# Kernel optimization log

Hardware: AMD Instinct MI355X
Metric: run time of the kernel (lower is better)

The kernel has to match this reference:

```python
import jax, jax.numpy as jnp
import numpy as np

EMBED_DIM = 2048
NUM_HEADS = 16
HEAD_DIM = EMBED_DIM // NUM_HEADS
SCALES = [(1, 1, 1), (1, 2, 2), (1, 4, 4), (1, 6, 6), (1, 8, 8),
          (1, 12, 12), (1, 16, 16), (1, 20, 20), (1, 24, 24), (1, 32, 32)]
LENS = [t * h * w for (t, h, w) in SCALES]
SEQ_LEN = int(np.sum(LENS))  # 2521
BATCH = 2
MAX_SCALE_MUL = float(np.log(100.0))


def _block_causal_bias():
    # VAR-style: queries in scale-block i attend to all keys up to end of block i.
    cum = np.cumsum(LENS)
    q_end = np.repeat(cum, LENS)                      # [L] visible kv length per query
    visible = np.arange(SEQ_LEN)[None, :] < q_end[:, None]
    bias = np.where(visible, 0.0, -np.inf).astype(np.float32)
    return jnp.asarray(bias)[None, None]              # [1,1,L,L]


def setup_inputs() -> dict:
    key = jax.random.key(0)
    ks = jax.random.split(key, 8)
    C, H, hd, L, B = EMBED_DIM, NUM_HEADS, HEAD_DIM, SEQ_LEN, BATCH
    x = jax.random.normal(ks[0], (B, L, C), dtype=jnp.float32)
    W_qkv = jax.random.normal(ks[1], (3 * C, C), dtype=jnp.float32) * (1.0 / np.sqrt(C))
    q_bias = jnp.zeros((C,), jnp.float32)
    v_bias = jnp.zeros((C,), jnp.float32)
    scale_mul_log = jnp.full((1, H, 1, 1), np.log(4.0), jnp.float32)
    proj_W = jax.random.normal(ks[2], (C, C), dtype=jnp.float32) * (1.0 / np.sqrt(C))
    proj_b = jnp.zeros((C,), jnp.float32)
    # 2D RoPE cache, pre-sliced for scale_ind=0: (2,1,1,1,L,hd//2) = (cos, sin)
    angles = jax.random.uniform(ks[3], (L, hd // 2), dtype=jnp.float32, maxval=2.0 * np.pi)
    rope_cache = jnp.stack([jnp.cos(angles), jnp.sin(angles)])[:, None, None, None]
    attn_bias = _block_causal_bias()
    return {"x": x, "W_qkv": W_qkv, "q_bias": q_bias, "v_bias": v_bias,
            "scale_mul_log": scale_mul_log, "proj_W": proj_W, "proj_b": proj_b,
            "rope_cache": rope_cache, "attn_bias": attn_bias}


def _l2norm(t, eps=1e-12):
    # torch F.normalize: x / max(||x||_2, eps)
    n = jnp.sqrt(jnp.sum(t * t, axis=-1, keepdims=True))
    return t / jnp.maximum(n, eps)


def reference(x, W_qkv, q_bias, v_bias, scale_mul_log, proj_W, proj_b, rope_cache, attn_bias):
    B, L, C = x.shape
    H, hd = NUM_HEADS, HEAD_DIM
    bias = jnp.concatenate([q_bias, jnp.zeros_like(q_bias), v_bias])
    qkv = x @ W_qkv.T + bias                               # [B,L,3C]
    qkv = qkv.reshape(B, L, 3, H, hd).transpose(2, 0, 3, 1, 4)  # [3,B,H,L,hd]
    q, k, v = qkv[0], qkv[1], qkv[2]
    # cosine attention: L2-norm q,k; q scaled by clamped learnable per-head scale
    scale_mul = jnp.exp(jnp.minimum(scale_mul_log, MAX_SCALE_MUL))
    q = _l2norm(q) * scale_mul
    k = _l2norm(k)
    # 2D RoPE applied jointly to q and k
    qk = jnp.stack([q, k]).reshape(2, B, H, L, hd // 2, 2)
    cos, sin = rope_cache[0], rope_cache[1]                # [1,1,1,L,hd//2]
    re = cos * qk[..., 0] - sin * qk[..., 1]
    im = sin * qk[..., 0] + cos * qk[..., 1]
    qk = jnp.stack([re, im], axis=-1).reshape(2, B, H, L, hd)
    q, k = qk[0], qk[1]
    # SDPA with scale=1 (cos_attn) and additive block-causal bias
    scores = jnp.einsum('bhqd,bhkd->bhqk', q, k) + attn_bias
    attn = jax.nn.softmax(scores, axis=-1)
    out = jnp.einsum('bhqk,bhkd->bhqd', attn, v)           # [B,H,L,hd]
    out = out.transpose(0, 2, 1, 3).reshape(B, L, C)
    return out @ proj_W.T + proj_b
```

## Files before the change

### kernel.cpp

```cpp
#include <hip/hip_runtime.h>
#include <stdint.h>

#define SEQL 2521
#define LPAD 2560
#define NB 2
#define NH 16
#define HD 128
#define CD 2048
#define KD 2048

typedef float f32x4 __attribute__((ext_vector_type(4)));
typedef __bf16 bf16x8 __attribute__((ext_vector_type(8)));
typedef unsigned short u16x8 __attribute__((ext_vector_type(8)));

static __device__ __forceinline__ unsigned short bf16c(float f){
  __bf16 h = (__bf16)f;
  return __builtin_bit_cast(unsigned short, h);
}
static __device__ __forceinline__ float bf2f(unsigned short s){
  union { unsigned u; float f; } v; v.u = ((unsigned)s) << 16; return v.f;
}
static __device__ __forceinline__ bf16x8 asbf(u16x8 v){ return __builtin_bit_cast(bf16x8, v); }

typedef const __attribute__((address_space(1))) unsigned int* gas1_t;
typedef __attribute__((address_space(3))) unsigned int* las3_t;
static __device__ __forceinline__ void glds16(const void* g, void* l){
  __builtin_amdgcn_global_load_lds((gas1_t)g, (las3_t)l, 16, 0, 0);
}

__global__ __launch_bounds__(256) void prep_kernel(
    const float* __restrict__ x, const float* __restrict__ wqkv, const float* __restrict__ projw,
    unsigned short* __restrict__ xb, unsigned short* __restrict__ wb, unsigned short* __restrict__ pw)
{
  const int NX = (NB*LPAD*CD)/4;
  const int NW = (3*CD*CD)/4;
  const int NPj = (CD*CD)/4;
  const int total = NX + NW + NPj;
  for (int v = blockIdx.x*256 + threadIdx.x; v < total; v += gridDim.x*256){
    if (v < NX){
      int e = v << 2;
      int row = e >> 11, col = e & 2047;
      int b = (row >= LPAD) ? 1 : 0;
      int l = row - b*LPAD;
      ushort4 o;
      if (l < SEQL){
        const float4 f = *(const float4*)(x + (((long)(b*SEQL + l)) << 11) + col);
        o.x = bf16c(f.x); o.y = bf16c(f.y); o.z = bf16c(f.z); o.w = bf16c(f.w);
      } else { o.x = 0; o.y = 0; o.z = 0; o.w = 0; }
      *(ushort4*)(xb + e) = o;
    } else if (v < NX + NW){
      long i = (long)(v - NX) << 2;
      const float4 f = *(const float4*)(wqkv + i);
      ushort4 o; o.x=bf16c(f.x); o.y=bf16c(f.y); o.z=bf16c(f.z); o.w=bf16c(f.w);
      *(ushort4*)(wb + i) = o;
    } else {
      long i = (long)(v - NX - NW) << 2;
      const float4 f = *(const float4*)(projw + i);
      ushort4 o; o.x=bf16c(f.x); o.y=bf16c(f.y); o.z=bf16c(f.z); o.w=bf16c(f.w);
      *(ushort4*)(pw + i) = o;
    }
  }
}

static __device__ __forceinline__ void gemm_core(
    const unsigned short* __restrict__ A, const unsigned short* __restrict__ Bm,
    unsigned short* As, unsigned short* Bs, int m0, int n0, f32x4 acc[4][4])
{
  const int tid = threadIdx.x;
  const int w = tid >> 6, lane = tid & 63;
  const int g = lane >> 4, lr = lane & 15;
  const int wm = w >> 1, wn = w & 1;
  const unsigned short* aS0 = A + (long)(m0 + (tid >> 2))*KD + ((tid & 3) << 3);
  const unsigned short* aS1 = aS0 + (long)64*KD;
  const unsigned short* bS0 = Bm + (long)(n0 + (tid >> 2))*KD + ((tid & 3) << 3);
  const unsigned short* bS1 = bS0 + (long)64*KD;
  unsigned short* aD0 = As + (w << 9);
  unsigned short* aD1 = As + 2048 + (w << 9);
  unsigned short* bD0 = Bs + (w << 9);
  unsigned short* bD1 = Bs + 2048 + (w << 9);
  const unsigned short* aRd = As + ((wm << 6) + lr)*32 + (g << 3);
  const unsigned short* bRd = Bs + ((wn << 6) + lr)*32 + (g << 3);
  for (int kt = 0; kt < KD/32; ++kt){
    __syncthreads();
    const int ko = kt << 5;
    glds16(aS0 + ko, aD0);
    glds16(aS1 + ko, aD1);
    glds16(bS0 + ko, bD0);
    glds16(bS1 + ko, bD1);
    __syncthreads();
    u16x8 af[4], bfr[4];
#pragma unroll
    for (int i = 0; i < 4; ++i) af[i]  = *(const u16x8*)(aRd + i*16*32);
#pragma unroll
    for (int j = 0; j < 4; ++j) bfr[j] = *(const u16x8*)(bRd + j*16*32);
#pragma unroll
    for (int i = 0; i < 4; ++i)
#pragma unroll
      for (int j = 0; j < 4; ++j)
        acc[i][j] = __builtin_amdgcn_mfma_f32_16x16x32_bf16(asbf(af[i]), asbf(bfr[j]), acc[i][j], 0, 0, 0);
  }
}

__global__ __launch_bounds__(256) void gemm_qkv(
    const unsigned short* __restrict__ A, const unsigned short* __restrict__ W,
    const float* __restrict__ qb, const float* __restrict__ vb,
    unsigned short* __restrict__ qg, unsigned short* __restrict__ kg,
    unsigned short* __restrict__ vt)
{
  __shared__ __align__(16) unsigned short As[128*32];
  __shared__ __align__(16) unsigned short Bs[128*32];
  f32x4 acc[4][4] = {};
  const int m0 = blockIdx.x << 7, n0 = blockIdx.y << 7;
  gemm_core(A, W, As, Bs, m0, n0, acc);
  const int tid = threadIdx.x;
  const int w = tid >> 6, lane = tid & 63, g = lane >> 4, lr = lane & 15;
  const int wm = w >> 1, wn = w & 1;
  const int part = n0 >> 11;
  const int b = (m0 >= LPAD) ? 1 : 0;
  const int l0 = m0 - b*LPAD;
  const int hb = (n0 & 2047) >> 7;
#pragma unroll
  for (int ai = 0; ai < 4; ++ai){
#pragma unroll
    for (int bj = 0; bj < 4; ++bj){
      const int d = (wn << 6) + (bj << 4) + lr;
      const int mloc = (wm << 6) + (ai << 4) + (g << 2);
      const float bias = (part == 0) ? qb[(hb << 7) + d] : ((part == 2) ? vb[(hb << 7) + d] : 0.f);
      const f32x4 v = acc[ai][bj];
      if (part == 2){
        ushort4 o;
        o.x = bf16c(v[0] + bias); o.y = bf16c(v[1] + bias);
        o.z = bf16c(v[2] + bias); o.w = bf16c(v[3] + bias);
        *(ushort4*)(vt + ((long)((b*NH + hb)*HD + d))*LPAD + l0 + mloc) = o;
      } else {
        unsigned short* dst = (part ? kg : qg) + (((long)(b*NH + hb)*LPAD) + l0 + mloc)*HD + d;
        dst[0]     = bf16c(v[0] + bias);
        dst[HD]    = bf16c(v[1] + bias);
        dst[2*HD]  = bf16c(v[2] + bias);
        dst[3*HD]  = bf16c(v[3] + bias);
      }
    }
  }
}

__global__ __launch_bounds__(256) void gemm_proj(
    const unsigned short* __restrict__ A, const unsigned short* __restrict__ W,
    const float* __restrict__ pbias, float* __restrict__ out)
{
  __shared__ __align__(16) unsigned short As[128*32];
  __shared__ __align__(16) unsigned short Bs[128*32];
  f32x4 acc[4][4] = {};
  const int m0 = blockIdx.x << 7, n0 = blockIdx.y << 7;
  gemm_core(A, W, As, Bs, m0, n0, acc);
  const int tid = threadIdx.x;
  const int w = tid >> 6, lane = tid & 63, g = lane >> 4, lr = lane & 15;
  const int wm = w >> 1, wn = w & 1;
  const int b = (m0 >= LPAD) ? 1 : 0;
  const int l0 = m0 - b*LPAD;
#pragma unroll
  for (int ai = 0; ai < 4; ++ai){
#pragma unroll
    for (int bj = 0; bj < 4; ++bj){
      const int n = n0 + (wn << 6) + (bj << 4) + lr;
      const int mloc = (wm << 6) + (ai << 4) + (g << 2);
      const float bias = pbias[n];
      const f32x4 v = acc[ai][bj];
#pragma unroll
      for (int r = 0; r < 4; ++r){
        const int l = l0 + mloc + r;
        if (l < SEQL) out[(((long)b*SEQL + l) << 11) + n] = v[r] + bias;
      }
    }
  }
}

__global__ __launch_bounds__(256) void rope_norm(
    unsigned short* __restrict__ qg, unsigned short* __restrict__ kg,
    const float* __restrict__ rope, const float* __restrict__ smlog)
{
  const int sub = threadIdx.x & 15;
  const int l = blockIdx.x*16 + (threadIdx.x >> 4);
  if (l >= SEQL) return;
  const int pb = blockIdx.y;
  const int part = pb >> 5, bh = pb & 31, h = bh & 15;
  unsigned short* base = (part ? kg : qg) + ((long)bh*LPAD + l)*HD + (sub << 3);
  const u16x8 v = *(const u16x8*)base;
  float f[8];
#pragma unroll
  for (int i = 0; i < 8; ++i) f[i] = bf2f(v[i]);
  float ss = 0.f;
#pragma unroll
  for (int i = 0; i < 8; ++i) ss += f[i]*f[i];
  ss += __shfl_xor(ss, 1, 16);
  ss += __shfl_xor(ss, 2, 16);
  ss += __shfl_xor(ss, 4, 16);
  ss += __shfl_xor(ss, 8, 16);
  float inv = 1.f / fmaxf(sqrtf(ss), 1e-12f);
  if (part == 0){
    float sl = fminf(smlog[h], 4.605170185988091f);
    inv *= __expf(sl) * 1.4426950408889634f;
  }
  const float4 cs = *(const float4*)(rope + (long)l*64 + (sub << 2));
  const float4 sn = *(const float4*)(rope + (long)(SEQL + l)*64 + (sub << 2));
  u16x8 o;
  const float c4[4] = {cs.x, cs.y, cs.z, cs.w};
  const float s4[4] = {sn.x, sn.y, sn.z, sn.w};
#pragma unroll
  for (int p = 0; p < 4; ++p){
    const float re = f[2*p], im = f[2*p+1];
    o[2*p]   = bf16c((c4[p]*re - s4[p]*im)*inv);
    o[2*p+1] = bf16c((s4[p]*re + c4[p]*im)*inv);
  }
  *(u16x8*)base = o;
}

static __device__ __forceinline__ int q_end_of(int q){
  if (q >= SEQL) return 1;
  if (q < 121){
    if (q < 1) return 1;
    if (q < 5) return 5;
    if (q < 21) return 21;
    if (q < 57) return 57;
    return 121;
  }
  if (q < 265) return 265;
  if (q < 521) return 521;
  if (q < 921) return 921;
  if (q < 1497) return 1497;
  return 2521;
}

__global__ __launch_bounds__(512) void attn_kernel(
    const unsigned short* __restrict__ qg, const unsigned short* __restrict__ kg,
    const unsigned short* __restrict__ vt, unsigned short* __restrict__ aout)
{
  __shared__ __align__(16) unsigned short Ks[64*128];
  __shared__ __align__(16) unsigned short Vs[128*64];
  __shared__ __align__(16) unsigned short Ps[8][16*72];
  const int tid = threadIdx.x, w = tid >> 6, lane = tid & 63;
  const int g = lane >> 4, lr = lane & 15;
  const int qt = (int)gridDim.x - 1 - (int)blockIdx.x;
  const int bh = blockIdx.y;
  const int q0 = qt << 7, qw = q0 + (w << 4);
  const long kvBase = (long)bh * LPAD * HD;

  u16x8 qf[4];
  {
    const unsigned short* qrow = qg + kvBase + (long)(qw + lr)*HD + (g << 3);
#pragma unroll
    for (int c = 0; c < 4; ++c) qf[c] = *(const u16x8*)(qrow + (c << 5));
  }
  const int qe  = q_end_of(qw + lr);
  const int qe0 = q_end_of(qw);
  const int qmax = (q0 + 127 < SEQL - 1) ? q0 + 127 : SEQL - 1;
  const int nt = (q_end_of(qmax) + 63) >> 6;

  float m2 = -1e30f, l_run = 0.f;
  f32x4 acco[8] = {};

  for (int t = 0; t < nt; ++t){
    __syncthreads();
    const int kvb = t << 6;
#pragma unroll
    for (int c = 0; c < 2; ++c){
      const int idx = (c << 9) + tid;
      const int kv = idx >> 4, ch = idx & 15;
      glds16(kg + kvBase + (long)(kvb + kv)*HD + ((ch ^ (kv & 7)) << 3),
             Ks + (c << 12) + (w << 9));
      const int dd = idx >> 3, ch2 = idx & 7;
      glds16(vt + kvBase + (long)dd*LPAD + kvb + ((ch2 ^ (dd & 7)) << 3),
             Vs + (c << 12) + (w << 9));
    }
    __syncthreads();

    f32x4 accs[4] = {};
    __builtin_amdgcn_s_setprio(1);
#pragma unroll
    for (int mf = 0; mf < 4; ++mf){
      const int kvr = (mf << 4) + lr;
      const unsigned short* krow = Ks + kvr*HD;
      const int sw = kvr & 7;
#pragma unroll
      for (int c = 0; c < 4; ++c){
        u16x8 kf = *(const u16x8*)(krow + ((((c << 2) + g) ^ sw) << 3));
        accs[mf] = __builtin_amdgcn_mfma_f32_16x16x32_bf16(asbf(kf), asbf(qf[c]), accs[mf], 0, 0, 0);
      }
    }
    __builtin_amdgcn_s_setprio(0);

    float tmax = -1e30f;
    if (kvb + 64 <= qe0){
#pragma unroll
      for (int mf = 0; mf < 4; ++mf)
#pragma unroll
        for (int r = 0; r < 4; ++r) tmax = fmaxf(tmax, accs[mf][r]);
    } else {
#pragma unroll
      for (int mf = 0; mf < 4; ++mf){
#pragma unroll
        for (int r = 0; r < 4; ++r){
          const int kvg = kvb + (mf << 4) + (g << 2) + r;
          float s = (kvg < qe) ? accs[mf][r] : -1e30f;
          accs[mf][r] = s;
          tmax = fmaxf(tmax, s);
        }
      }
    }
    tmax = fmaxf(tmax, __shfl_xor(tmax, 16, 64));
    tmax = fmaxf(tmax, __shfl_xor(tmax, 32, 64));

    float alpha = 1.f;
    const bool need = !__all(tmax <= m2 + 11.0f);
    if (need){
      const float mnew = fmaxf(m2, tmax);
      alpha = exp2f(m2 - mnew);
      m2 = mnew;
      const float a0 = __shfl(alpha, (g << 2) + 0, 64);
      const float a1 = __shfl(alpha, (g << 2) + 1, 64);
      const float a2 = __shfl(alpha, (g << 2) + 2, 64);
      const float a3 = __shfl(alpha, (g << 2) + 3, 64);
#pragma unroll
      for (int nf = 0; nf < 8; ++nf){
        acco[nf][0] *= a0; acco[nf][1] *= a1; acco[nf][2] *= a2; acco[nf][3] *= a3;
      }
    }

    float tsum = 0.f;
#pragma unroll
    for (int mf = 0; mf < 4; ++mf){
#pragma unroll
      for (int r = 0; r < 4; ++r){
        const float p = exp2f(accs[mf][r] - m2);
        accs[mf][r] = p;
        tsum += p;
      }
    }
    tsum += __shfl_xor(tsum, 16, 64);
    tsum += __shfl_xor(tsum, 32, 64);
    l_run = l_run*alpha + tsum;

    unsigned short* prow = &Ps[w][lr*72 + (g << 2)];
#pragma unroll
    for (int mf = 0; mf < 4; ++mf){
      uint2 pk;
      pk.x = (unsigned)bf16c(accs[mf][0]) | ((unsigned)bf16c(accs[mf][1]) << 16);
      pk.y = (unsigned)bf16c(accs[mf][2]) | ((unsigned)bf16c(accs[mf][3]) << 16);
      *(uint2*)(prow + (mf << 4)) = pk;
    }

    __builtin_amdgcn_s_setprio(1);
#pragma unroll
    for (int c = 0; c < 2; ++c){
      u16x8 pf = *(const u16x8*)(&Ps[w][lr*72 + (c << 5) + (g << 3)]);
      const int sw2 = lr & 7;
#pragma unroll
      for (int nf = 0; nf < 8; ++nf){
        u16x8 vf = *(const u16x8*)(Vs + ((nf << 4) + lr)*64 + ((((c << 2) + g) ^ sw2) << 3));
        acco[nf] = __builtin_amdgcn_mfma_f32_16x16x32_bf16(asbf(pf), asbf(vf), acco[nf], 0, 0, 0);
      }
    }
    __builtin_amdgcn_s_setprio(0);
  }

  const float rcp = 1.f / l_run;
  const float li0 = __shfl(rcp, (g << 2) + 0, 64);
  const float li1 = __shfl(rcp, (g << 2) + 1, 64);
  const float li2 = __shfl(rcp, (g << 2) + 2, 64);
  const float li3 = __shfl(rcp, (g << 2) + 3, 64);
  const int b = bh >> 4, h = bh & 15;
#pragma unroll
  for (int r = 0; r < 4; ++r){
    const int qq = qw + (g << 2) + r;
    if (qq < SEQL){
      const float lir = (r == 0) ? li0 : ((r == 1) ? li1 : ((r == 2) ? li2 : li3));
      unsigned short* dst = aout + (((long)(b*LPAD + qq)) << 11) + (h << 7) + lr;
#pragma unroll
      for (int nf = 0; nf < 8; ++nf)
        dst[nf << 4] = bf16c(acco[nf][r] * lir);
    }
  }
}

extern "C" void kernel_launch(void* const* d_in, const int* in_sizes, int n_in,
                              void* d_out, int out_size, void* d_ws, size_t ws_size,
                              hipStream_t stream) {
  const float* x     = (const float*)d_in[0];
  const float* wqkv  = (const float*)d_in[1];
  const float* qb    = (const float*)d_in[2];
  const float* vb    = (const float*)d_in[3];
  const float* smlog = (const float*)d_in[4];
  const float* projw = (const float*)d_in[5];
  const float* projb = (const float*)d_in[6];
  const float* rope  = (const float*)d_in[7];
  float* out = (float*)d_out;

  unsigned short* xb = (unsigned short*)d_ws;
  unsigned short* wb = xb + (size_t)NB*LPAD*CD;
  unsigned short* pw = wb + (size_t)3*CD*CD;
  unsigned short* qg = pw + (size_t)CD*CD;
  unsigned short* kg = qg + (size_t)NB*NH*LPAD*HD;
  unsigned short* vt = kg + (size_t)NB*NH*LPAD*HD;

  prep_kernel<<<2048, 256, 0, stream>>>(x, wqkv, projw, xb, wb, pw);
  gemm_qkv<<<dim3(40, 48), 256, 0, stream>>>(xb, wb, qb, vb, qg, kg, vt);
  rope_norm<<<dim3(158, 64), 256, 0, stream>>>(qg, kg, rope, smlog);
  attn_kernel<<<dim3(20, 32), 512, 0, stream>>>(qg, kg, vt, xb);
  gemm_proj<<<dim3(40, 16), 256, 0, stream>>>(xb, pw, projb, out);
}
```

Before: 574.2 us.

## Rewrite QKV and projection GEMMs as 256x256 double-buffered pipelined 8-wave kernels

Replaces the simple 128x128 GEMM core, which issues two block-wide barriers per 32-wide k step, with a 256x256-tile, 512-thread kernel. It uses a double-buffered 64-wide k stage, XOR-swizzled LDS layout, interleaved global-to-LDS loads between MFMA phases, and s_setprio around the MFMA bursts. A swizzled 1D block index groups neighbouring tiles for L2 reuse. The aim is to hide load latency and raise MFMA utilisation, at the cost of 128KB LDS per block, large accumulators, and fewer blocks (160 for proj), which may cut occupancy and wave-level parallelism.

```diff
diff --git a/kernel.cpp b/kernel.cpp
--- a/kernel.cpp
+++ b/kernel.cpp
@@ -62,78 +62,154 @@
   }
 }
 
-static __device__ __forceinline__ void gemm_core(
+static __device__ __forceinline__ void gemm8p(
     const unsigned short* __restrict__ A, const unsigned short* __restrict__ Bm,
-    unsigned short* As, unsigned short* Bs, int m0, int n0, f32x4 acc[4][4])
+    unsigned short* lds, int m0, int n0, f32x4 acc[8][4])
 {
   const int tid = threadIdx.x;
   const int w = tid >> 6, lane = tid & 63;
   const int g = lane >> 4, lr = lane & 15;
-  const int wm = w >> 1, wn = w & 1;
-  const unsigned short* aS0 = A + (long)(m0 + (tid >> 2))*KD + ((tid & 3) << 3);
-  const unsigned short* aS1 = aS0 + (long)64*KD;
-  const unsigned short* bS0 = Bm + (long)(n0 + (tid >> 2))*KD + ((tid & 3) << 3);
-  const unsigned short* bS1 = bS0 + (long)64*KD;
-  unsigned short* aD0 = As + (w << 9);
-  unsigned short* aD1 = As + 2048 + (w << 9);
-  unsigned short* bD0 = Bs + (w << 9);
-  unsigned short* bD1 = Bs + 2048 + (w << 9);
-  const unsigned short* aRd = As + ((wm << 6) + lr)*32 + (g << 3);
-  const unsigned short* bRd = Bs + ((wn << 6) + lr)*32 + (g << 3);
-  for (int kt = 0; kt < KD/32; ++kt){
-    __syncthreads();
-    const int ko = kt << 5;
-    glds16(aS0 + ko, aD0);
-    glds16(aS1 + ko, aD1);
-    glds16(bS0 + ko, bD0);
-    glds16(bS1 + ko, bD1);
-    __syncthreads();
-    u16x8 af[4], bfr[4];
-#pragma unroll
-    for (int i = 0; i < 4; ++i) af[i]  = *(const u16x8*)(aRd + i*16*32);
-#pragma unroll
-    for (int j = 0; j < 4; ++j) bfr[j] = *(const u16x8*)(bRd + j*16*32);
-#pragma unroll
-    for (int i = 0; i < 4; ++i)
-#pragma unroll
-      for (int j = 0; j < 4; ++j)
-        acc[i][j] = __builtin_amdgcn_mfma_f32_16x16x32_bf16(asbf(af[i]), asbf(bfr[j]), acc[i][j], 0, 0, 0);
-  }
-}
-
-__global__ __launch_bounds__(256) void gemm_qkv(
+  const int wm = w >> 2, wn = w & 3;
+  const int xorv = (lr & 7) << 3;
+  const int off0 = (g << 3) ^ xorv;
+  const int arow = wm*128 + lr;
+  const int brow = wn*64 + lr;
+
+  auto stage = [&](int mat, int kt, int half, int buf){
+    const unsigned short* G = mat ? Bm : A;
+    const int base0 = mat ? n0 : m0;
+    unsigned short* lb = lds + buf*32768 + mat*16384;
+#pragma unroll
+    for (int p = 0; p < 2; ++p){
+      const int cb_ = (half<<10) + (p<<9) + (w<<6);
+      const int c = cb_ + lane;
+      const int row = c >> 3, cc = c & 7;
+      glds16(G + (size_t)(base0 + row)*KD + (kt<<6) + ((cc ^ (row & 7)) << 3),
+             lb + (cb_ << 3));
+    }
+  };
+  auto rdA = [&](int buf, int i, int ks)->u16x8 {
+    return *(const u16x8*)(lds + buf*32768 + (arow + i*16)*64 + (off0 ^ (ks<<5)));
+  };
+  auto rdB = [&](int buf, int j, int ks)->u16x8 {
+    return *(const u16x8*)(lds + buf*32768 + 16384 + (brow + j*16)*64 + (off0 ^ (ks<<5)));
+  };
+
+  u16x8 bfr[4][2], af[2][2];
+  auto mfma16 = [&](int q){
+#pragma unroll
+    for (int i2 = 0; i2 < 2; ++i2)
+#pragma unroll
+      for (int ks = 0; ks < 2; ++ks)
+#pragma unroll
+        for (int j = 0; j < 4; ++j)
+          acc[2*q+i2][j] = __builtin_amdgcn_mfma_f32_16x16x32_bf16(
+              asbf(af[i2][ks]), asbf(bfr[j][ks]), acc[2*q+i2][j], 0, 0, 0);
+  };
+
+#define PH_SYNC_MFMA(Q) \
+    __builtin_amdgcn_s_barrier(); \
+    asm volatile("s_waitcnt lgkmcnt(0)" ::: "memory"); \
+    __builtin_amdgcn_s_setprio(1); mfma16(Q); __builtin_amdgcn_s_setprio(0);
+
+  stage(0, 0, 0, 0); stage(0, 0, 1, 0);
+  stage(1, 0, 0, 0); stage(1, 0, 1, 0);
+  stage(1, 1, 0, 1); stage(1, 1, 1, 1);
+  asm volatile("s_waitcnt vmcnt(4)" ::: "memory");
+  __builtin_amdgcn_s_barrier();
+
+  const int NI = KD >> 7;
+  for (int it = 0; it < NI; ++it){
+    const int kt = it << 1;
+    const bool last = (it == NI-1);
+#pragma unroll
+    for (int j = 0; j < 4; ++j){ bfr[j][0]=rdB(0,j,0); bfr[j][1]=rdB(0,j,1); }
+    af[0][0]=rdA(0,0,0); af[0][1]=rdA(0,0,1); af[1][0]=rdA(0,1,0); af[1][1]=rdA(0,1,1);
+    stage(0, kt+1, 0, 1);
+    PH_SYNC_MFMA(0)
+    __builtin_amdgcn_s_barrier();
+
+    af[0][0]=rdA(0,2,0); af[0][1]=rdA(0,2,1); af[1][0]=rdA(0,3,0); af[1][1]=rdA(0,3,1);
+    stage(0, kt+1, 1, 1);
+    PH_SYNC_MFMA(1)
+    __builtin_amdgcn_s_barrier();
+
+    af[0][0]=rdA(0,4,0); af[0][1]=rdA(0,4,1); af[1][0]=rdA(0,5,0); af[1][1]=rdA(0,5,1);
+    if (!last) stage(1, kt+2, 0, 0);
+    PH_SYNC_MFMA(2)
+    __builtin_amdgcn_s_barrier();
+
+    af[0][0]=rdA(0,6,0); af[0][1]=rdA(0,6,1); af[1][0]=rdA(0,7,0); af[1][1]=rdA(0,7,1);
+    if (!last) stage(1, kt+2, 1, 0);
+    PH_SYNC_MFMA(3)
+    if (last) { asm volatile("s_waitcnt vmcnt(0)" ::: "memory"); }
+    else      { asm volatile("s_waitcnt vmcnt(4)" ::: "memory"); }
+    __builtin_amdgcn_s_barrier();
+
+#pragma unroll
+    for (int j = 0; j < 4; ++j){ bfr[j][0]=rdB(1,j,0); bfr[j][1]=rdB(1,j,1); }
+    af[0][0]=rdA(1,0,0); af[0][1]=rdA(1,0,1); af[1][0]=rdA(1,1,0); af[1][1]=rdA(1,1,1);
+    if (!last) stage(0, kt+2, 0, 0);
+    PH_SYNC_MFMA(0)
+    __builtin_amdgcn_s_barrier();
+
+    af[0][0]=rdA(1,2,0); af[0][1]=rdA(1,2,1); af[1][0]=rdA(1,3,0); af[1][1]=rdA(1,3,1);
+    if (!last) stage(0, kt+2, 1, 0);
+    PH_SYNC_MFMA(1)
+    __builtin_amdgcn_s_barrier();
+
+    af[0][0]=rdA(1,4,0); af[0][1]=rdA(1,4,1); af[1][0]=rdA(1,5,0); af[1][1]=rdA(1,5,1);
+    if (!last) stage(1, kt+3, 0, 1);
+    PH_SYNC_MFMA(2)
+    __builtin_amdgcn_s_barrier();
+
+    af[0][0]=rdA(1,6,0); af[0][1]=rdA(1,6,1); af[1][0]=rdA(1,7,0); af[1][1]=rdA(1,7,1);
+    if (!last) stage(1, kt+3, 1, 1);
+    PH_SYNC_MFMA(3)
+    if (last) { asm volatile("s_waitcnt vmcnt(0)" ::: "memory"); }
+    else      { asm volatile("s_waitcnt vmcnt(4)" ::: "memory"); }
+    __builtin_amdgcn_s_barrier();
+  }
+#undef PH_SYNC_MFMA
+}
+
+__global__ __launch_bounds__(512, 2) void gemm_qkv(
     const unsigned short* __restrict__ A, const unsigned short* __restrict__ W,
     const float* __restrict__ qb, const float* __restrict__ vb,
     unsigned short* __restrict__ qg, unsigned short* __restrict__ kg,
     unsigned short* __restrict__ vt)
 {
-  __shared__ __align__(16) unsigned short As[128*32];
-  __shared__ __align__(16) unsigned short Bs[128*32];
-  f32x4 acc[4][4] = {};
-  const int m0 = blockIdx.x << 7, n0 = blockIdx.y << 7;
-  gemm_core(A, W, As, Bs, m0, n0, acc);
+  __shared__ __align__(16) unsigned short lds[65536];
+  f32x4 acc[8][4] = {};
+  const int bid = blockIdx.x;
+  const int swz = (bid & 7)*60 + (bid >> 3);
+  const int mt = swz / 24, ntt = swz % 24;
+  const int m0 = mt << 8, n0 = ntt << 8;
+  gemm8p(A, W, lds, m0, n0, acc);
+
   const int tid = threadIdx.x;
   const int w = tid >> 6, lane = tid & 63, g = lane >> 4, lr = lane & 15;
-  const int wm = w >> 1, wn = w & 1;
+  const int wm = w >> 2, wn = w & 3;
   const int part = n0 >> 11;
   const int b = (m0 >= LPAD) ? 1 : 0;
   const int l0 = m0 - b*LPAD;
-  const int hb = (n0 & 2047) >> 7;
-#pragma unroll
-  for (int ai = 0; ai < 4; ++ai){
-#pragma unroll
-    for (int bj = 0; bj < 4; ++bj){
-      const int d = (wn << 6) + (bj << 4) + lr;
-      const int mloc = (wm << 6) + (ai << 4) + (g << 2);
-      const float bias = (part == 0) ? qb[(hb << 7) + d] : ((part == 2) ? vb[(hb << 7) + d] : 0.f);
-      const f32x4 v = acc[ai][bj];
+  const int colbase = (n0 & 2047) + wn*64;
+#pragma unroll
+  for (int i = 0; i < 8; ++i){
+    const int mloc = wm*128 + i*16 + (g << 2);
+#pragma unroll
+    for (int j = 0; j < 4; ++j){
+      const int col = colbase + j*16 + lr;
+      const int hb = col >> 7, d = col & 127;
+      const float bias = (part == 0) ? qb[col] : ((part == 2) ? vb[col] : 0.f);
+      const f32x4 v = acc[i][j];
       if (part == 2){
         ushort4 o;
         o.x = bf16c(v[0] + bias); o.y = bf16c(v[1] + bias);
         o.z = bf16c(v[2] + bias); o.w = bf16c(v[3] + bias);
-        *(ushort4*)(vt + ((long)((b*NH + hb)*HD + d))*LPAD + l0 + mloc) = o;
+        *(ushort4*)(vt + ((size_t)((b*NH + hb)*HD + d))*LPAD + l0 + mloc) = o;
       } else {
-        unsigned short* dst = (part ? kg : qg) + (((long)(b*NH + hb)*LPAD) + l0 + mloc)*HD + d;
+        unsigned short* dst = (part ? kg : qg) + (((size_t)(b*NH + hb)*LPAD) + l0 + mloc)*HD + d;
         dst[0]     = bf16c(v[0] + bias);
         dst[HD]    = bf16c(v[1] + bias);
         dst[2*HD]  = bf16c(v[2] + bias);
@@ -143,32 +219,35 @@
   }
 }
 
-__global__ __launch_bounds__(256) void gemm_proj(
+__global__ __launch_bounds__(512, 2) void gemm_proj(
     const unsigned short* __restrict__ A, const unsigned short* __restrict__ W,
     const float* __restrict__ pbias, float* __restrict__ out)
 {
-  __shared__ __align__(16) unsigned short As[128*32];
-  __shared__ __align__(16) unsigned short Bs[128*32];
-  f32x4 acc[4][4] = {};
-  const int m0 = blockIdx.x << 7, n0 = blockIdx.y << 7;
-  gemm_core(A, W, As, Bs, m0, n0, acc);
+  __shared__ __align__(16) unsigned short lds[65536];
+  f32x4 acc[8][4] = {};
+  const int bid = blockIdx.x;
+  const int swz = (bid & 7)*20 + (bid >> 3);
+  const int mt = swz >> 3, ntt = swz & 7;
+  const int m0 = mt << 8, n0 = ntt << 8;
+  gemm8p(A, W, lds, m0, n0, acc);
+
   const int tid = threadIdx.x;
   const int w = tid >> 6, lane = tid & 63, g = lane >> 4, lr = lane & 15;
-  const int wm = w >> 1, wn = w & 1;
+  const int wm = w >> 2, wn = w & 3;
   const int b = (m0 >= LPAD) ? 1 : 0;
   const int l0 = m0 - b*LPAD;
 #pragma unroll
-  for (int ai = 0; ai < 4; ++ai){
-#pragma unroll
-    for (int bj = 0; bj < 4; ++bj){
-      const int n = n0 + (wn << 6) + (bj << 4) + lr;
-      const int mloc = (wm << 6) + (ai << 4) + (g << 2);
+  for (int i = 0; i < 8; ++i){
+    const int mloc = wm*128 + i*16 + (g << 2);
+#pragma unroll
+    for (int j = 0; j < 4; ++j){
+      const int n = n0 + wn*64 + j*16 + lr;
       const float bias = pbias[n];
-      const f32x4 v = acc[ai][bj];
+      const f32x4 v = acc[i][j];
 #pragma unroll
       for (int r = 0; r < 4; ++r){
         const int l = l0 + mloc + r;
-        if (l < SEQL) out[(((long)b*SEQL + l) << 11) + n] = v[r] + bias;
+        if (l < SEQL) out[(((size_t)(b*SEQL + l)) << 11) + n] = v[r] + bias;
       }
     }
   }
@@ -402,8 +481,8 @@
   unsigned short* vt = kg + (size_t)NB*NH*LPAD*HD;
 
   prep_kernel<<<2048, 256, 0, stream>>>(x, wqkv, projw, xb, wb, pw);
-  gemm_qkv<<<dim3(40, 48), 256, 0, stream>>>(xb, wb, qb, vb, qg, kg, vt);
+  gemm_qkv<<<480, 512, 0, stream>>>(xb, wb, qb, vb, qg, kg, vt);
   rope_norm<<<dim3(158, 64), 256, 0, stream>>>(qg, kg, rope, smlog);
   attn_kernel<<<dim3(20, 32), 512, 0, stream>>>(qg, kg, vt, xb);
-  gemm_proj<<<dim3(40, 16), 256, 0, stream>>>(xb, pw, projb, out);
-}
+  gemm_proj<<<160, 512, 0, stream>>>(xb, pw, projb, out);
+}
```

After: 535.3 us. -6.8%, faster.
